# Performance work log

Measured on AMD Instinct MI355X. Metric: run time of the kernel, lower is better.

## Reference

```python
import jax, jax.numpy as jnp
import numpy as np

B, N, D_SIM = 4096, 64, 768
NLI_DIM = 768
KK = 5
H1, NUM_CLASSES = 1024, 4


def setup_inputs() -> dict:
    key = jax.random.key(0)
    ks = jax.random.split(key, 8)
    sim_stance_emb = jax.random.normal(ks[0], (B, D_SIM), dtype=jnp.float32)
    nli_stance_emb = jax.random.normal(ks[1], (B, NLI_DIM), dtype=jnp.float32)
    sim_body_emb = jax.random.normal(ks[2], (B, N, D_SIM), dtype=jnp.float32)
    nli_body_emb = jax.random.normal(ks[3], (B, N, NLI_DIM), dtype=jnp.float32)
    fan1 = (KK + 1) * NLI_DIM
    W1 = jax.random.uniform(ks[4], (H1, fan1), jnp.float32, -1.0, 1.0) / jnp.sqrt(fan1)
    b1 = jax.random.uniform(ks[5], (H1,), jnp.float32, -1.0, 1.0) / jnp.sqrt(fan1)
    W2 = jax.random.uniform(ks[6], (NUM_CLASSES, H1), jnp.float32, -1.0, 1.0) / jnp.sqrt(H1)
    b2 = jax.random.uniform(ks[7], (NUM_CLASSES,), jnp.float32, -1.0, 1.0) / jnp.sqrt(H1)
    return {"sim_stance_emb": sim_stance_emb, "nli_stance_emb": nli_stance_emb,
            "sim_body_emb": sim_body_emb, "nli_body_emb": nli_body_emb,
            "W1": W1, "b1": b1, "W2": W2, "b2": b2}


def reference(sim_stance_emb, nli_stance_emb, sim_body_emb, nli_body_emb, W1, b1, W2, b2):
    # sims[b, n] = <sim_stance_emb[b], sim_body_emb[b, n]>  (bmm + squeeze)
    sims = jnp.einsum('bd,bnd->bn', sim_stance_emb, sim_body_emb)
    _, top_idx = jax.lax.top_k(sims, KK)                      # [B, KK]
    # gather top-k nli body sentence embeddings: [B, KK, NLI_DIM]
    top_emb = jnp.take_along_axis(nli_body_emb, top_idx[:, :, None], axis=1)
    xx = jnp.concatenate([nli_stance_emb, top_emb.reshape(top_emb.shape[0], -1)], axis=1)
    xx = jax.nn.relu(xx @ W1.T + b1)
    return xx @ W2.T + b2
```

## Files before the change

kernel.cpp:

```cpp
#include <hip/hip_runtime.h>
#include <stdint.h>
#include <stddef.h>

#define B_N   4096
#define NSENT 64
#define DDIM  768
#define TOPK  5
#define FAN1  4608
#define H1DIM 1024
#define NCLS  4
#define KDIM  4608

typedef __attribute__((ext_vector_type(8))) __bf16 bf16x8;
typedef __attribute__((ext_vector_type(4))) float  f32x4;

__device__ __forceinline__ unsigned short f2bf(float f) {
    unsigned int u = __float_as_uint(f);
    unsigned int r = (u + 0x7fffu + ((u >> 16) & 1u)) >> 16;
    return (unsigned short)r;
}

__device__ __forceinline__ void gl_lds16(const void* g, void* l) {
    __builtin_amdgcn_global_load_lds((__attribute__((address_space(1))) void*)(g),
                                     (__attribute__((address_space(3))) void*)(l),
                                     16, 0, 0);
}

__global__ __launch_bounds__(256) void k_topk_gather(
    const float* __restrict__ sim_stance,
    const float* __restrict__ sim_body,
    const float* __restrict__ nli_stance,
    const float* __restrict__ nli_body,
    unsigned short* __restrict__ xx)
{
    const int b    = blockIdx.x;
    const int tid  = threadIdx.x;
    const int lane = tid & 63;
    const int wave = tid >> 6;
    __shared__ float sims[NSENT];
    __shared__ int   topidx[TOPK];

    const float4* st4 = (const float4*)(sim_stance + (size_t)b * DDIM);
    const float4  s0 = st4[lane], s1 = st4[64 + lane], s2 = st4[128 + lane];

    const float* bodyb = sim_body + (size_t)b * NSENT * DDIM;
    for (int n = wave; n < NSENT; n += 4) {
        const float4* r4 = (const float4*)(bodyb + (size_t)n * DDIM);
        float4 a = r4[lane], c = r4[64 + lane], e = r4[128 + lane];
        float p = a.x*s0.x + a.y*s0.y + a.z*s0.z + a.w*s0.w
                + c.x*s1.x + c.y*s1.y + c.z*s1.z + c.w*s1.w
                + e.x*s2.x + e.y*s2.y + e.z*s2.z + e.w*s2.w;
        #pragma unroll
        for (int off = 32; off; off >>= 1) p += __shfl_xor(p, off);
        if (lane == 0) sims[n] = p;
    }
    __syncthreads();

    if (wave == 0) {
        float v = sims[lane];
        #pragma unroll
        for (int k = 0; k < TOPK; ++k) {
            float bv = v; int bi = lane;
            #pragma unroll
            for (int off = 32; off; off >>= 1) {
                float ov = __shfl_xor(bv, off);
                int   oi = __shfl_xor(bi, off);
                if (ov > bv || (ov == bv && oi < bi)) { bv = ov; bi = oi; }
            }
            if (lane == 0) topidx[k] = bi;
            if (lane == bi) v = -3.402823466e38f;
        }
    }
    __syncthreads();

    unsigned short* xrow = xx + (size_t)b * FAN1;
    for (int task = tid; task < 1152; task += 256) {
        const int seg = task / 192;
        const int t   = task - seg * 192;
        const float* src = (seg == 0)
            ? (nli_stance + (size_t)b * DDIM)
            : (nli_body + ((size_t)b * NSENT + topidx[seg - 1]) * DDIM);
        float4 v = ((const float4*)src)[t];
        ushort4 o;
        o.x = f2bf(v.x); o.y = f2bf(v.y); o.z = f2bf(v.z); o.w = f2bf(v.w);
        ((ushort4*)(xrow + seg * DDIM))[t] = o;
    }
}

__global__ __launch_bounds__(256) void k_f32_to_bf16x4(
    const float* __restrict__ in, unsigned short* __restrict__ o, int n4)
{
    int i = blockIdx.x * 256 + threadIdx.x;
    if (i < n4) {
        float4 v = ((const float4*)in)[i];
        ushort4 r;
        r.x = f2bf(v.x); r.y = f2bf(v.y); r.z = f2bf(v.z); r.w = f2bf(v.w);
        ((ushort4*)o)[i] = r;
    }
}

__global__ __launch_bounds__(256, 2) void k_gemm1(
    const unsigned short* __restrict__ A,
    const unsigned short* __restrict__ W,
    const float* __restrict__ bias,
    float* __restrict__ Hd)
{
    constexpr int BM = 128, BN = 64, BK = 64;
    constexpr int K = KDIM;
    __shared__ unsigned short lA[BM * BK];
    __shared__ unsigned short lB[BN * BK];

    const int tid = threadIdx.x, lane = tid & 63, wave = tid >> 6;
    const int bn = blockIdx.x & 15, bm = blockIdx.x >> 4;
    const int wm = wave >> 1, wn = wave & 1;

    const int q   = wave * 64 + lane;
    const int q8  = q >> 3;
    const int sc  = (q & 7) ^ (q8 & 7);
    const unsigned short* gA[4];
    const unsigned short* gB[2];
    #pragma unroll
    for (int j = 0; j < 4; ++j)
        gA[j] = A + (size_t)(bm * BM + j * 32 + q8) * K + sc * 8;
    #pragma unroll
    for (int j = 0; j < 2; ++j)
        gB[j] = W + (size_t)(bn * BN + j * 32 + q8) * K + sc * 8;
    unsigned short* lAd[4];
    unsigned short* lBd[2];
    #pragma unroll
    for (int j = 0; j < 4; ++j) lAd[j] = &lA[(j * 256 + wave * 64) * 8];
    #pragma unroll
    for (int j = 0; j < 2; ++j) lBd[j] = &lB[(j * 256 + wave * 64) * 8];

    const int r16 = lane & 15;
    const int x   = r16 & 7;
    const int p0  = (lane >> 4) ^ x;
    const int p1  = p0 ^ 4;
    const unsigned short* paBase = &lA[(wm * 64 + r16) * BK];
    const unsigned short* pbBase = &lB[(wn * 32 + r16) * BK];

    f32x4 acc[4][2];
    #pragma unroll
    for (int m = 0; m < 4; ++m)
        #pragma unroll
        for (int n = 0; n < 2; ++n) acc[m][n] = {0.f, 0.f, 0.f, 0.f};

    for (int kt = 0; kt < K / BK; ++kt) {
        #pragma unroll
        for (int j = 0; j < 4; ++j) { gl_lds16(gA[j], lAd[j]); gA[j] += BK; }
        #pragma unroll
        for (int j = 0; j < 2; ++j) { gl_lds16(gB[j], lBd[j]); gB[j] += BK; }
        __syncthreads();

        bf16x8 fa[4][2], fb[2][2];
        #pragma unroll
        for (int m = 0; m < 4; ++m) {
            fa[m][0] = *(const bf16x8*)(paBase + m * 16 * BK + p0 * 8);
            fa[m][1] = *(const bf16x8*)(paBase + m * 16 * BK + p1 * 8);
        }
        #pragma unroll
        for (int n = 0; n < 2; ++n) {
            fb[n][0] = *(const bf16x8*)(pbBase + n * 16 * BK + p0 * 8);
            fb[n][1] = *(const bf16x8*)(pbBase + n * 16 * BK + p1 * 8);
        }
        #pragma unroll
        for (int h = 0; h < 2; ++h)
            #pragma unroll
            for (int m = 0; m < 4; ++m)
                #pragma unroll
                for (int n = 0; n < 2; ++n)
                    acc[m][n] = __builtin_amdgcn_mfma_f32_16x16x32_bf16(
                        fa[m][h], fb[n][h], acc[m][n], 0, 0, 0);
        __syncthreads();
    }

    const int colbase = bn * BN + wn * 32 + r16;
    const int rowbase = bm * BM + wm * 64 + (lane >> 4) * 4;
    #pragma unroll
    for (int n = 0; n < 2; ++n) {
        const int col = colbase + n * 16;
        const float bv = bias[col];
        #pragma unroll
        for (int m = 0; m < 4; ++m) {
            const int row = rowbase + m * 16;
            #pragma unroll
            for (int j = 0; j < 4; ++j) {
                float v = acc[m][n][j] + bv;
                Hd[(size_t)(row + j) * H1DIM + col] = v > 0.f ? v : 0.f;
            }
        }
    }
}

__global__ __launch_bounds__(256) void k_gemm2(
    const float* __restrict__ Hd, const float* __restrict__ W2,
    const float* __restrict__ b2, float* __restrict__ out)
{
    __shared__ float w2s[NCLS * H1DIM];
    const int tid = threadIdx.x, lane = tid & 63, wave = tid >> 6;
    const int row = blockIdx.x * 4 + wave;
    for (int i = tid; i < NCLS * H1DIM; i += 256) w2s[i] = W2[i];
    __syncthreads();

    const float4* h4 = (const float4*)(Hd + (size_t)row * H1DIM);
    const float4* w0 = (const float4*)&w2s[0];
    const float4* w1 = (const float4*)&w2s[H1DIM];
    const float4* w2 = (const float4*)&w2s[2 * H1DIM];
    const float4* w3 = (const float4*)&w2s[3 * H1DIM];
    float a0 = 0.f, a1 = 0.f, a2 = 0.f, a3 = 0.f;
    #pragma unroll
    for (int j = 0; j < 4; ++j) {
        const int idx = j * 64 + lane;
        float4 h = h4[idx], xv;
        xv = w0[idx]; a0 += h.x*xv.x + h.y*xv.y + h.z*xv.z + h.w*xv.w;
        xv = w1[idx]; a1 += h.x*xv.x + h.y*xv.y + h.z*xv.z + h.w*xv.w;
        xv = w2[idx]; a2 += h.x*xv.x + h.y*xv.y + h.z*xv.z + h.w*xv.w;
        xv = w3[idx]; a3 += h.x*xv.x + h.y*xv.y + h.z*xv.z + h.w*xv.w;
    }
    #pragma unroll
    for (int off = 32; off; off >>= 1) {
        a0 += __shfl_xor(a0, off);
        a1 += __shfl_xor(a1, off);
        a2 += __shfl_xor(a2, off);
        a3 += __shfl_xor(a3, off);
    }
    if (lane == 0) {
        float* o = out + (size_t)row * NCLS;
        o[0] = a0 + b2[0]; o[1] = a1 + b2[1]; o[2] = a2 + b2[2]; o[3] = a3 + b2[3];
    }
}

extern "C" void kernel_launch(void* const* d_in, const int* in_sizes, int n_in,
                              void* d_out, int out_size, void* d_ws, size_t ws_size,
                              hipStream_t stream)
{
    const float* sim_stance = (const float*)d_in[0];
    const float* nli_stance = (const float*)d_in[1];
    const float* sim_body   = (const float*)d_in[2];
    const float* nli_body   = (const float*)d_in[3];
    const float* W1 = (const float*)d_in[4];
    const float* b1 = (const float*)d_in[5];
    const float* W2 = (const float*)d_in[6];
    const float* b2 = (const float*)d_in[7];
    float* out = (float*)d_out;

    char* ws = (char*)d_ws;
    unsigned short* xx     = (unsigned short*)ws;
    unsigned short* w1b    = (unsigned short*)(ws + 37748736u);
    float*          hidden = (float*)(ws + 37748736u + 9437184u);

    k_f32_to_bf16x4<<<dim3(4608), dim3(256), 0, stream>>>(W1, w1b, 1179648);
    k_topk_gather<<<dim3(B_N), dim3(256), 0, stream>>>(sim_stance, sim_body,
                                                       nli_stance, nli_body, xx);
    k_gemm1<<<dim3(512), dim3(256), 0, stream>>>(xx, w1b, b1, hidden);
    k_gemm2<<<dim3(1024), dim3(256), 0, stream>>>(hidden, W2, b2, out);
}
```

Baseline: 277.2 us.

## Double-buffer LDS tiles in GEMM1 to overlap global loads with MFMA

Splits the A and B shared-memory tiles of the first GEMM into two buffers. The loop now issues the global-to-LDS loads for the next K tile before running the MFMA work on the current one, with a prologue and epilogue covering all 72 K tiles. This aims to hide global-load latency behind matrix compute and removes one barrier per K step. In exchange, LDS use per block doubles to 48 KB, which could limit occupancy, and the loop is unrolled in fixed pairs tied to K.

New measurement: 299.5 us. 8.0% more time.

```diff
diff --git a/kernel.cpp b/kernel.cpp
--- a/kernel.cpp
+++ b/kernel.cpp
@@ -107,8 +107,8 @@
 {
     constexpr int BM = 128, BN = 64, BK = 64;
     constexpr int K = KDIM;
-    __shared__ unsigned short lA[BM * BK];
-    __shared__ unsigned short lB[BN * BK];
+    __shared__ unsigned short lA[2][BM * BK];
+    __shared__ unsigned short lB[2][BN * BK];
 
     const int tid = threadIdx.x, lane = tid & 63, wave = tid >> 6;
     const int bn = blockIdx.x & 15, bm = blockIdx.x >> 4;
@@ -125,19 +125,13 @@
     #pragma unroll
     for (int j = 0; j < 2; ++j)
         gB[j] = W + (size_t)(bn * BN + j * 32 + q8) * K + sc * 8;
-    unsigned short* lAd[4];
-    unsigned short* lBd[2];
-    #pragma unroll
-    for (int j = 0; j < 4; ++j) lAd[j] = &lA[(j * 256 + wave * 64) * 8];
-    #pragma unroll
-    for (int j = 0; j < 2; ++j) lBd[j] = &lB[(j * 256 + wave * 64) * 8];
+    const int ldsOff = (wave * 64) * 8;
 
     const int r16 = lane & 15;
-    const int x   = r16 & 7;
-    const int p0  = (lane >> 4) ^ x;
+    const int p0  = (lane >> 4) ^ (r16 & 7);
     const int p1  = p0 ^ 4;
-    const unsigned short* paBase = &lA[(wm * 64 + r16) * BK];
-    const unsigned short* pbBase = &lB[(wn * 32 + r16) * BK];
+    const int aRowOff = (wm * 64 + r16) * BK;
+    const int bRowOff = (wn * 32 + r16) * BK;
 
     f32x4 acc[4][2];
     #pragma unroll
@@ -145,34 +139,51 @@
         #pragma unroll
         for (int n = 0; n < 2; ++n) acc[m][n] = {0.f, 0.f, 0.f, 0.f};
 
-    for (int kt = 0; kt < K / BK; ++kt) {
-        #pragma unroll
-        for (int j = 0; j < 4; ++j) { gl_lds16(gA[j], lAd[j]); gA[j] += BK; }
-        #pragma unroll
-        for (int j = 0; j < 2; ++j) { gl_lds16(gB[j], lBd[j]); gB[j] += BK; }
-        __syncthreads();
-
-        bf16x8 fa[4][2], fb[2][2];
-        #pragma unroll
-        for (int m = 0; m < 4; ++m) {
-            fa[m][0] = *(const bf16x8*)(paBase + m * 16 * BK + p0 * 8);
-            fa[m][1] = *(const bf16x8*)(paBase + m * 16 * BK + p1 * 8);
-        }
-        #pragma unroll
-        for (int n = 0; n < 2; ++n) {
-            fb[n][0] = *(const bf16x8*)(pbBase + n * 16 * BK + p0 * 8);
-            fb[n][1] = *(const bf16x8*)(pbBase + n * 16 * BK + p1 * 8);
-        }
-        #pragma unroll
-        for (int h = 0; h < 2; ++h)
-            #pragma unroll
-            for (int m = 0; m < 4; ++m)
-                #pragma unroll
-                for (int n = 0; n < 2; ++n)
-                    acc[m][n] = __builtin_amdgcn_mfma_f32_16x16x32_bf16(
-                        fa[m][h], fb[n][h], acc[m][n], 0, 0, 0);
-        __syncthreads();
-    }
+#define STAGE(SEL) do {                                                     \
+    _Pragma("unroll")                                                       \
+    for (int j = 0; j < 4; ++j) {                                           \
+        gl_lds16(gA[j], &lA[SEL][j * 2048 + ldsOff]); gA[j] += BK;          \
+    }                                                                       \
+    _Pragma("unroll")                                                       \
+    for (int j = 0; j < 2; ++j) {                                           \
+        gl_lds16(gB[j], &lB[SEL][j * 2048 + ldsOff]); gB[j] += BK;          \
+    }                                                                       \
+} while (0)
+
+#define COMPUTE(SEL) do {                                                   \
+    bf16x8 fa[4][2], fb[2][2];                                              \
+    _Pragma("unroll")                                                       \
+    for (int m = 0; m < 4; ++m) {                                           \
+        fa[m][0] = *(const bf16x8*)(&lA[SEL][aRowOff + m * 16 * BK + p0 * 8]); \
+        fa[m][1] = *(const bf16x8*)(&lA[SEL][aRowOff + m * 16 * BK + p1 * 8]); \
+    }                                                                       \
+    _Pragma("unroll")                                                       \
+    for (int n = 0; n < 2; ++n) {                                           \
+        fb[n][0] = *(const bf16x8*)(&lB[SEL][bRowOff + n * 16 * BK + p0 * 8]); \
+        fb[n][1] = *(const bf16x8*)(&lB[SEL][bRowOff + n * 16 * BK + p1 * 8]); \
+    }                                                                       \
+    _Pragma("unroll")                                                       \
+    for (int h = 0; h < 2; ++h)                                             \
+        _Pragma("unroll")                                                   \
+        for (int m = 0; m < 4; ++m)                                         \
+            _Pragma("unroll")                                               \
+            for (int n = 0; n < 2; ++n)                                     \
+                acc[m][n] = __builtin_amdgcn_mfma_f32_16x16x32_bf16(        \
+                    fa[m][h], fb[n][h], acc[m][n], 0, 0, 0);                \
+} while (0)
+
+    STAGE(0);
+    __syncthreads();
+    #pragma unroll 1
+    for (int it = 0; it < 35; ++it) {
+        STAGE(1); COMPUTE(0); __syncthreads();
+        STAGE(0); COMPUTE(1); __syncthreads();
+    }
+    STAGE(1); COMPUTE(0); __syncthreads();
+    COMPUTE(1);
+
+#undef STAGE
+#undef COMPUTE
 
     const int colbase = bn * BN + wn * 32 + r16;
     const int rowbase = bm * BM + wm * 64 + (lane >> 4) * 4;
```

## Process four body rows per wave in sims dot product and remap GEMM block order

Applied to the files above, without the earlier changes.

In the top-k kernel, each wave now splits into four 16-lane groups that each compute one sentence similarity. Each lane keeps 12 float4s of the stance vector in registers, so the loop runs 4 iterations instead of 16 and the reduction needs 4 shuffle steps instead of 6, giving more loads in flight per iteration. The GEMM1 kernel remaps blockIdx so that consecutive block IDs are spread across XCD-sized groups, aiming for better L2 locality on the multi-XCD chip. The register use for the stance vector rises, which could lower occupancy.

Measured after the change: 274.5 us. Within noise of the previous version (-1.0%).

```diff
diff --git a/kernel.cpp b/kernel.cpp
--- a/kernel.cpp
+++ b/kernel.cpp
@@ -37,22 +37,30 @@
     const int tid  = threadIdx.x;
     const int lane = tid & 63;
     const int wave = tid >> 6;
+    const int g    = lane >> 4;
+    const int c    = lane & 15;
     __shared__ float sims[NSENT];
     __shared__ int   topidx[TOPK];
 
     const float4* st4 = (const float4*)(sim_stance + (size_t)b * DDIM);
-    const float4  s0 = st4[lane], s1 = st4[64 + lane], s2 = st4[128 + lane];
+    float4 st[12];
+    #pragma unroll
+    for (int j = 0; j < 12; ++j) st[j] = st4[c + 16 * j];
 
     const float* bodyb = sim_body + (size_t)b * NSENT * DDIM;
-    for (int n = wave; n < NSENT; n += 4) {
-        const float4* r4 = (const float4*)(bodyb + (size_t)n * DDIM);
-        float4 a = r4[lane], c = r4[64 + lane], e = r4[128 + lane];
-        float p = a.x*s0.x + a.y*s0.y + a.z*s0.z + a.w*s0.w
-                + c.x*s1.x + c.y*s1.y + c.z*s1.z + c.w*s1.w
-                + e.x*s2.x + e.y*s2.y + e.z*s2.z + e.w*s2.w;
-        #pragma unroll
-        for (int off = 32; off; off >>= 1) p += __shfl_xor(p, off);
-        if (lane == 0) sims[n] = p;
+    #pragma unroll 1
+    for (int it = 0; it < 4; ++it) {
+        const int r = wave * 16 + it * 4 + g;
+        const float4* r4 = (const float4*)(bodyb + (size_t)r * DDIM);
+        float p = 0.f;
+        #pragma unroll
+        for (int j = 0; j < 12; ++j) {
+            float4 v = r4[c + 16 * j];
+            p += v.x*st[j].x + v.y*st[j].y + v.z*st[j].z + v.w*st[j].w;
+        }
+        #pragma unroll
+        for (int off = 8; off; off >>= 1) p += __shfl_xor(p, off);
+        if (c == 0) sims[r] = p;
     }
     __syncthreads();
 
@@ -111,7 +119,9 @@
     __shared__ unsigned short lB[BN * BK];
 
     const int tid = threadIdx.x, lane = tid & 63, wave = tid >> 6;
-    const int bn = blockIdx.x & 15, bm = blockIdx.x >> 4;
+    const int bid = blockIdx.x;
+    const int wk  = (bid & 7) * 64 + (bid >> 3);
+    const int bn  = wk & 15, bm = wk >> 4;
     const int wm = wave >> 1, wn = wave & 1;
 
     const int q   = wave * 64 + lane;
@@ -133,8 +143,7 @@
     for (int j = 0; j < 2; ++j) lBd[j] = &lB[(j * 256 + wave * 64) * 8];
 
     const int r16 = lane & 15;
-    const int x   = r16 & 7;
-    const int p0  = (lane >> 4) ^ x;
+    const int p0  = (lane >> 4) ^ (r16 & 7);
     const int p1  = p0 ^ 4;
     const unsigned short* paBase = &lA[(wm * 64 + r16) * BK];
     const unsigned short* pbBase = &lB[(wn * 32 + r16) * BK];
```
